# Optimization experiments

Hardware: AMD Instinct MI355X
Metric: run time of the kernel (lower is better)

## Reference

```python
import jax, jax.numpy as jnp
import numpy as np

BETA = 0.25

def setup_inputs() -> dict:
    key = jax.random.key(0)
    k1, k2 = jax.random.split(key)
    x = jax.random.normal(k1, (32, 32, 32, 64), dtype=jnp.float32)
    # tf.random_uniform_initializer default: uniform in [-0.05, 0.05]
    embeddings = jax.random.uniform(k2, (64, 1024), dtype=jnp.float32,
                                    minval=-0.05, maxval=0.05)
    return {"x": x, "embeddings": embeddings}

def reference(x, embeddings):
    D, K = embeddings.shape
    flat = x.reshape(-1, D)                                   # [N, D]
    # squared L2 distances to each codebook vector (expanded form)
    sim = flat @ embeddings                                   # [N, K]
    dists = (jnp.sum(flat * flat, axis=1, keepdims=True)
             + jnp.sum(embeddings * embeddings, axis=0)
             - 2.0 * sim)                                     # [N, K]
    idx = jnp.argmin(dists, axis=1)                           # [N]
    quantized = embeddings.T[idx].reshape(x.shape)            # gather == one-hot matmul
    commitment_loss = BETA * jnp.mean((jax.lax.stop_gradient(quantized) - x) ** 2)
    codebook_loss = jnp.mean((quantized - jax.lax.stop_gradient(x)) ** 2)
    loss = commitment_loss + codebook_loss
    out = x + jax.lax.stop_gradient(quantized - x)            # straight-through
    return out, loss
```

## Files before the change

### kernel.cpp

```cpp
#include <hip/hip_runtime.h>
#include <hip/hip_bf16.h>


#define NROWS 32768
#define DDIM  64
#define KCODE 1024
#define NELEM (NROWS * DDIM)
#define MARGIN 4e-3f
#define FIXBLOCKS 256
#define MAINBLK 256

typedef __attribute__((ext_vector_type(8))) _Float16 f16x8;
typedef __attribute__((ext_vector_type(4))) float f32x4;

static __device__ __forceinline__ unsigned short f2h(float v) {
    _Float16 h = (_Float16)v;
    unsigned short b;
    __builtin_memcpy(&b, &h, 2);
    return b;
}
static __device__ __forceinline__ void gload16(const void* g, void* l) {
    __builtin_amdgcn_global_load_lds(
        (const __attribute__((address_space(1))) void*)g,
        (__attribute__((address_space(3))) void*)l, 16, 0, 0);
}

__global__ void vq_prep(const float* __restrict__ e,
                        float* __restrict__ se,
                        float* __restrict__ eT,
                        unsigned short* __restrict__ ehSw,
                        int* __restrict__ ctrl) {
    __shared__ float tile[64][17];
    const int t = threadIdx.x;
    const int k0 = blockIdx.x * 16;
    if (blockIdx.x == 0 && t < 4) ctrl[t] = 0;
    #pragma unroll
    for (int i = 0; i < 4; ++i) {
        int idx = i * 256 + t;
        int d = idx >> 4, kk = idx & 15;
        tile[d][kk] = e[d * KCODE + k0 + kk];
    }
    __syncthreads();
    if (t < 16) {
        float s = 0.f;
        #pragma unroll
        for (int d = 0; d < 64; ++d) { float v = tile[d][t]; s = fmaf(v, v, s); }
        se[k0 + t] = s;
    }
    const int kk = t >> 4;
    const int dg = (t & 15) * 4;
    const int kg = k0 + kk;
    float v0 = tile[dg + 0][kk], v1 = tile[dg + 1][kk];
    float v2 = tile[dg + 2][kk], v3 = tile[dg + 3][kk];
    *(float4*)&eT[(size_t)kg * 64 + dg] = make_float4(v0, v1, v2, v3);
    const int sw = (((dg >> 3) ^ (kg & 7)) << 3) + (dg & 7);
    *(ushort4*)&ehSw[(size_t)kg * 64 + sw] =
        make_ushort4(f2h(v0), f2h(v1), f2h(v2), f2h(v3));
}

__launch_bounds__(512)
__global__ void vq_main(const float* __restrict__ x,
                        const float* __restrict__ se,
                        const float* __restrict__ eT,
                        const unsigned short* __restrict__ ehSw,
                        float* __restrict__ out,
                        float* __restrict__ parts,
                        int* __restrict__ cnt,
                        int2* __restrict__ list) {
    __shared__ unsigned short Beh[KCODE * 64];
    __shared__ float sse[KCODE];
    __shared__ float wsum[8];

    const int t = threadIdx.x;
    const int lane = t & 63;
    const int w = t >> 6;
    const int quad = lane >> 4, l15 = lane & 15;
    const int rowBase = blockIdx.x * 128 + w * 16;

    {
        const unsigned char* g = (const unsigned char*)ehSw;
        #pragma unroll
        for (int r = 0; r < 16; ++r)
            gload16(g + (size_t)(r * 512 + t) * 16, &Beh[(r * 512 + t) * 8]);
        float2 s2 = ((const float2*)se)[t];
        sse[2 * t + 0] = s2.x;
        sse[2 * t + 1] = s2.y;
    }

    f16x8 ah0, ah1, al0, al1;
    {
        const float4* ap0 = (const float4*)(x + (size_t)(rowBase + l15) * 64 + quad * 8);
        const float4* ap1 = (const float4*)(x + (size_t)(rowBase + l15) * 64 + 32 + quad * 8);
        float4 a0 = ap0[0], a1 = ap0[1], b0 = ap1[0], b1 = ap1[1];
        float av[8] = {a0.x, a0.y, a0.z, a0.w, a1.x, a1.y, a1.z, a1.w};
        float bv[8] = {b0.x, b0.y, b0.z, b0.w, b1.x, b1.y, b1.z, b1.w};
        f16x8 h0, h1, l0, l1;
        #pragma unroll
        for (int j = 0; j < 8; ++j) {
            _Float16 ha = (_Float16)av[j];
            _Float16 hb = (_Float16)bv[j];
            h0[j] = ha;
            h1[j] = hb;
            l0[j] = (_Float16)(av[j] - (float)ha);
            l1[j] = (_Float16)(bv[j] - (float)hb);
        }
        ah0 = h0; ah1 = h1; al0 = l0; al1 = l1;
    }
    __syncthreads();

    float sb[4], sb2[4];
    int   si[4];
    #pragma unroll
    for (int r = 0; r < 4; ++r) { sb[r] = 3.4e38f; sb2[r] = 3.4e38f; si[r] = 0; }

    const int slot0 = ((quad ^ (l15 & 7)) << 3);
    const int slot1 = (((quad + 4) ^ (l15 & 7)) << 3);

    #pragma unroll 4
    for (int nt = 0; nt < 64; ++nt) {
        const int code = nt * 16 + l15;
        f16x8 b0 = *(const f16x8*)&Beh[code * 64 + slot0];
        f16x8 b1 = *(const f16x8*)&Beh[code * 64 + slot1];
        float cse = sse[code];
        f32x4 aA = {0.f, 0.f, 0.f, 0.f}, aB = {0.f, 0.f, 0.f, 0.f};
        aA = __builtin_amdgcn_mfma_f32_16x16x32_f16(ah0, b0, aA, 0, 0, 0);
        aB = __builtin_amdgcn_mfma_f32_16x16x32_f16(ah1, b1, aB, 0, 0, 0);
        aA = __builtin_amdgcn_mfma_f32_16x16x32_f16(al0, b0, aA, 0, 0, 0);
        aB = __builtin_amdgcn_mfma_f32_16x16x32_f16(al1, b1, aB, 0, 0, 0);
        #pragma unroll
        for (int r = 0; r < 4; ++r) {
            float key = fmaf(-2.f, aA[r] + aB[r], cse);
            bool lt = key < sb[r];
            sb2[r] = fminf(sb2[r], fmaxf(sb[r], key));
            sb[r]  = fminf(sb[r], key);
            si[r]  = lt ? code : si[r];
        }
    }

    #pragma unroll
    for (int m = 1; m < 16; m <<= 1) {
        #pragma unroll
        for (int r = 0; r < 4; ++r) {
            float ob  = __shfl_xor(sb[r],  m, 64);
            float ob2 = __shfl_xor(sb2[r], m, 64);
            int   oi  = __shfl_xor(si[r],  m, 64);
            float nb2 = fminf(fminf(sb2[r], ob2), fmaxf(sb[r], ob));
            bool take = (ob < sb[r]) || (ob == sb[r] && oi < si[r]);
            sb[r] = take ? ob : sb[r];
            si[r] = take ? oi : si[r];
            sb2[r] = nb2;
        }
    }

    if (l15 == 0) {
        #pragma unroll
        for (int r = 0; r < 4; ++r) {
            if (sb2[r] - sb[r] < MARGIN) {
                int p = atomicAdd(cnt, 1);
                list[p] = make_int2(rowBase + quad * 4 + r, si[r]);
            }
        }
    }

    int src = (l15 >> 2) << 4;
    int j0 = __shfl(si[0], src, 64);
    int j1 = __shfl(si[1], src, 64);
    int j2 = __shfl(si[2], src, 64);
    int j3 = __shfl(si[3], src, 64);
    int rsel = l15 & 3;
    int myidx = rsel == 0 ? j0 : (rsel == 1 ? j1 : (rsel == 2 ? j2 : j3));

    {
        const float4* qrow = (const float4*)(eT + (size_t)myidx * 64 + quad * 16);
        const float4* xrow = (const float4*)(x + (size_t)(rowBase + l15) * 64 + quad * 16);
        float4* orow = (float4*)(out + (size_t)(rowBase + l15) * 64 + quad * 16);
        float lsum = 0.f;
        #pragma unroll
        for (int i = 0; i < 4; ++i) {
            float4 q = qrow[i];
            float4 xv = xrow[i];
            float4 o;
            float dx;
            dx = q.x - xv.x; o.x = xv.x + dx; lsum = fmaf(dx, dx, lsum);
            dx = q.y - xv.y; o.y = xv.y + dx; lsum = fmaf(dx, dx, lsum);
            dx = q.z - xv.z; o.z = xv.z + dx; lsum = fmaf(dx, dx, lsum);
            dx = q.w - xv.w; o.w = xv.w + dx; lsum = fmaf(dx, dx, lsum);
            orow[i] = o;
        }
        #pragma unroll
        for (int off = 32; off > 0; off >>= 1)
            lsum += __shfl_down(lsum, off, 64);
        if (lane == 0) wsum[w] = lsum;
    }
    __syncthreads();
    if (t == 0) {
        float s = 0.f;
        #pragma unroll
        for (int i = 0; i < 8; ++i) s += wsum[i];
        parts[blockIdx.x] = s;
    }
}

__launch_bounds__(256)
__global__ void vq_fix(const float* __restrict__ x,
                       const float* __restrict__ se,
                       const float* __restrict__ eT,
                       const int2* __restrict__ list,
                       const int* __restrict__ cnt,
                       const float* __restrict__ parts,
                       float* __restrict__ lossAcc,
                       int* __restrict__ done,
                       float* __restrict__ out) {
    __shared__ float xs[64];
    __shared__ float cb[256];
    __shared__ int   ci[256];
    __shared__ int   newIdxS;
    __shared__ int   lastS;
    const int t = threadIdx.x;
    const int n = *cnt;

    for (int i = blockIdx.x; i < n; i += gridDim.x) {
        int2 en = list[i];
        const int row = en.x, oldIdx = en.y;
        if (t < 64) xs[t] = x[(size_t)row * 64 + t];
        __syncthreads();

        float sx = 0.f;
        #pragma unroll
        for (int d = 0; d < 64; ++d) sx = fmaf(xs[d], xs[d], sx);

        const int k0 = t * 4;
        const float4* e0 = (const float4*)(eT + (size_t)(k0 + 0) * 64);
        const float4* e1 = (const float4*)(eT + (size_t)(k0 + 1) * 64);
        const float4* e2 = (const float4*)(eT + (size_t)(k0 + 2) * 64);
        const float4* e3 = (const float4*)(eT + (size_t)(k0 + 3) * 64);
        float dot0 = 0.f, dot1 = 0.f, dot2 = 0.f, dot3 = 0.f;
        #pragma unroll
        for (int i4 = 0; i4 < 16; ++i4) {
            float4 v0 = e0[i4], v1 = e1[i4], v2 = e2[i4], v3 = e3[i4];
            float xa = xs[4 * i4 + 0], xb = xs[4 * i4 + 1];
            float xc = xs[4 * i4 + 2], xd = xs[4 * i4 + 3];
            dot0 = fmaf(xa, v0.x, dot0); dot0 = fmaf(xb, v0.y, dot0);
            dot0 = fmaf(xc, v0.z, dot0); dot0 = fmaf(xd, v0.w, dot0);
            dot1 = fmaf(xa, v1.x, dot1); dot1 = fmaf(xb, v1.y, dot1);
            dot1 = fmaf(xc, v1.z, dot1); dot1 = fmaf(xd, v1.w, dot1);
            dot2 = fmaf(xa, v2.x, dot2); dot2 = fmaf(xb, v2.y, dot2);
            dot2 = fmaf(xc, v2.z, dot2); dot2 = fmaf(xd, v2.w, dot2);
            dot3 = fmaf(xa, v3.x, dot3); dot3 = fmaf(xb, v3.y, dot3);
            dot3 = fmaf(xc, v3.z, dot3); dot3 = fmaf(xd, v3.w, dot3);
        }
        float dd0 = (sx + se[k0 + 0]) - 2.0f * dot0;
        float dd1 = (sx + se[k0 + 1]) - 2.0f * dot1;
        float dd2 = (sx + se[k0 + 2]) - 2.0f * dot2;
        float dd3 = (sx + se[k0 + 3]) - 2.0f * dot3;
        float db = dd0; int di = k0;
        if (dd1 < db) { db = dd1; di = k0 + 1; }
        if (dd2 < db) { db = dd2; di = k0 + 2; }
        if (dd3 < db) { db = dd3; di = k0 + 3; }
        cb[t] = db; ci[t] = di;
        __syncthreads();

        if (t < 64) {
            float B = cb[t]; int I = ci[t];
            #pragma unroll
            for (int s = 64; s < 256; s += 64) {
                float b = cb[t + s]; int i2 = ci[t + s];
                bool take = (b < B) || (b == B && i2 < I);
                B = take ? b : B;
                I = take ? i2 : I;
            }
            #pragma unroll
            for (int m = 1; m < 64; m <<= 1) {
                float ob = __shfl_xor(B, m, 64);
                int   oi = __shfl_xor(I, m, 64);
                bool take = (ob < B) || (ob == B && oi < I);
                B = take ? ob : B;
                I = take ? oi : I;
            }
            if (t == 0) newIdxS = I;
        }
        __syncthreads();

        const int ni = newIdxS;
        if (ni != oldIdx) {
            if (t < 64) {
                float xv = xs[t];
                float qn = eT[(size_t)ni * 64 + t];
                float qo = eT[(size_t)oldIdx * 64 + t];
                float dn = qn - xv, dl = qo - xv;
                out[(size_t)row * 64 + t] = xv + dn;
                float delta = dn * dn - dl * dl;
                #pragma unroll
                for (int off = 32; off > 0; off >>= 1)
                    delta += __shfl_down(delta, off, 64);
                if (t == 0) atomicAdd(lossAcc, delta);
            }
        }
        __syncthreads();
    }

    if (t == 0) {
        __threadfence();
        int fin = atomicAdd(done, 1);
        lastS = (fin == FIXBLOCKS - 1) ? 1 : 0;
    }
    __syncthreads();
    if (lastS) {
        cb[t] = parts[t];
        __syncthreads();
        if (t < 64) {
            float v = cb[t] + cb[t + 64] + cb[t + 128] + cb[t + 192];
            #pragma unroll
            for (int off = 32; off > 0; off >>= 1)
                v += __shfl_down(v, off, 64);
            if (t == 0) {
                float total = v + atomicAdd(lossAcc, 0.0f);
                float m = total / (float)NELEM;
                out[NELEM] = 0.25f * m + m;
            }
        }
    }
}

extern "C" void kernel_launch(void* const* d_in, const int* in_sizes, int n_in,
                              void* d_out, int out_size, void* d_ws, size_t ws_size,
                              hipStream_t stream) {
    const float* x = (const float*)d_in[0];
    const float* e = (const float*)d_in[1];
    float* out = (float*)d_out;
    float* ws  = (float*)d_ws;

    float* lossAcc       = ws;
    int*   cnt           = (int*)(ws + 1);
    int*   done          = (int*)(ws + 2);
    float* se            = ws + 64;
    float* eT            = ws + 1280;
    unsigned short* ehSw = (unsigned short*)(ws + 66816);
    int2*  list          = (int2*)(ws + 99584);
    float* parts         = ws + 165120;

    vq_prep<<<64, 256, 0, stream>>>(e, se, eT, ehSw, (int*)ws);
    vq_main<<<MAINBLK, 512, 0, stream>>>(x, se, eT, ehSw, out, parts, cnt, list);
    vq_fix<<<FIXBLOCKS, 256, 0, stream>>>(x, se, eT, list, cnt, parts, lossAcc, done, out);
}
```

Before: 107.7 us.

## Fuse fp32 rescoring of ambiguous rows into main kernel, drop fix kernel

Ambiguous rows, where the fp16 top-2 gap is under the margin, are now rescored exactly in fp32 inside the main kernel. Each block keeps a shared-memory list of its flagged rows and resolves them before writing outputs, so the per-row write happens once with the final index. The separate fix kernel launch, the global atomic list and the loss-delta correction all go away. The cost is that flagged rows are handled serially within each block, with block-wide syncs per row, which may cause imbalance across blocks.

```diff
diff --git a/kernel.cpp b/kernel.cpp
--- a/kernel.cpp
+++ b/kernel.cpp
@@ -7,7 +7,6 @@
 #define KCODE 1024
 #define NELEM (NROWS * DDIM)
 #define MARGIN 4e-3f
-#define FIXBLOCKS 256
 #define MAINBLK 256
 
 typedef __attribute__((ext_vector_type(8))) _Float16 f16x8;
@@ -65,17 +64,26 @@
                         const unsigned short* __restrict__ ehSw,
                         float* __restrict__ out,
                         float* __restrict__ parts,
-                        int* __restrict__ cnt,
-                        int2* __restrict__ list) {
+                        int* __restrict__ done) {
     __shared__ unsigned short Beh[KCODE * 64];
     __shared__ float sse[KCODE];
+    __shared__ float cbuf[512];
+    __shared__ int   cibuf[512];
+    __shared__ int   rowIdx[128];
+    __shared__ int   flagRows[128];
+    __shared__ int   nFlag;
+    __shared__ float xs[64];
     __shared__ float wsum[8];
+    __shared__ int   lastS;
 
     const int t = threadIdx.x;
     const int lane = t & 63;
     const int w = t >> 6;
     const int quad = lane >> 4, l15 = lane & 15;
-    const int rowBase = blockIdx.x * 128 + w * 16;
+    const int rowBlk = blockIdx.x * 128;
+    const int rowBase = rowBlk + w * 16;
+
+    if (t == 0) { nFlag = 0; lastS = 0; }
 
     {
         const unsigned char* g = (const unsigned char*)ehSw;
@@ -155,23 +163,74 @@
     if (l15 == 0) {
         #pragma unroll
         for (int r = 0; r < 4; ++r) {
+            const int rl = w * 16 + quad * 4 + r;
+            rowIdx[rl] = si[r];
             if (sb2[r] - sb[r] < MARGIN) {
-                int p = atomicAdd(cnt, 1);
-                list[p] = make_int2(rowBase + quad * 4 + r, si[r]);
-            }
-        }
-    }
-
-    int src = (l15 >> 2) << 4;
-    int j0 = __shfl(si[0], src, 64);
-    int j1 = __shfl(si[1], src, 64);
-    int j2 = __shfl(si[2], src, 64);
-    int j3 = __shfl(si[3], src, 64);
-    int rsel = l15 & 3;
-    int myidx = rsel == 0 ? j0 : (rsel == 1 ? j1 : (rsel == 2 ? j2 : j3));
-
-    {
-        const float4* qrow = (const float4*)(eT + (size_t)myidx * 64 + quad * 16);
+                int p = atomicAdd(&nFlag, 1);
+                flagRows[p] = rl;
+            }
+        }
+    }
+    __syncthreads();
+
+    {
+        const int nf = nFlag;
+        for (int f = 0; f < nf; ++f) {
+            const int r = flagRows[f];
+            if (t < 64) xs[t] = x[(size_t)(rowBlk + r) * 64 + t];
+            __syncthreads();
+
+            float sx = 0.f;
+            #pragma unroll
+            for (int d = 0; d < 64; ++d) sx = fmaf(xs[d], xs[d], sx);
+
+            const int k0 = t * 2;
+            const float4* e0 = (const float4*)(eT + (size_t)(k0 + 0) * 64);
+            const float4* e1 = (const float4*)(eT + (size_t)(k0 + 1) * 64);
+            float dot0 = 0.f, dot1 = 0.f;
+            #pragma unroll
+            for (int i4 = 0; i4 < 16; ++i4) {
+                float4 v0 = e0[i4], v1 = e1[i4];
+                float xa = xs[4 * i4 + 0], xb = xs[4 * i4 + 1];
+                float xc = xs[4 * i4 + 2], xd = xs[4 * i4 + 3];
+                dot0 = fmaf(xa, v0.x, dot0); dot0 = fmaf(xb, v0.y, dot0);
+                dot0 = fmaf(xc, v0.z, dot0); dot0 = fmaf(xd, v0.w, dot0);
+                dot1 = fmaf(xa, v1.x, dot1); dot1 = fmaf(xb, v1.y, dot1);
+                dot1 = fmaf(xc, v1.z, dot1); dot1 = fmaf(xd, v1.w, dot1);
+            }
+            float dd0 = (sx + sse[k0 + 0]) - 2.0f * dot0;
+            float dd1 = (sx + sse[k0 + 1]) - 2.0f * dot1;
+            float db = dd0; int di = k0;
+            if (dd1 < db) { db = dd1; di = k0 + 1; }
+            cbuf[t] = db; cibuf[t] = di;
+            __syncthreads();
+
+            if (t < 64) {
+                float B = cbuf[t]; int I = cibuf[t];
+                #pragma unroll
+                for (int s = 64; s < 512; s += 64) {
+                    float b = cbuf[t + s]; int i2 = cibuf[t + s];
+                    bool take = (b < B) || (b == B && i2 < I);
+                    B = take ? b : B;
+                    I = take ? i2 : I;
+                }
+                #pragma unroll
+                for (int m = 1; m < 64; m <<= 1) {
+                    float ob = __shfl_xor(B, m, 64);
+                    int   oi = __shfl_xor(I, m, 64);
+                    bool take = (ob < B) || (ob == B && oi < I);
+                    B = take ? ob : B;
+                    I = take ? oi : I;
+                }
+                if (t == 0) rowIdx[r] = I;
+            }
+            __syncthreads();
+        }
+    }
+
+    {
+        const int idx = rowIdx[w * 16 + l15];
+        const float4* qrow = (const float4*)(eT + (size_t)idx * 64 + quad * 16);
         const float4* xrow = (const float4*)(x + (size_t)(rowBase + l15) * 64 + quad * 16);
         float4* orow = (float4*)(out + (size_t)(rowBase + l15) * 64 + quad * 16);
         float lsum = 0.f;
@@ -193,129 +252,27 @@
         if (lane == 0) wsum[w] = lsum;
     }
     __syncthreads();
+
     if (t == 0) {
         float s = 0.f;
         #pragma unroll
         for (int i = 0; i < 8; ++i) s += wsum[i];
         parts[blockIdx.x] = s;
-    }
-}
-
-__launch_bounds__(256)
-__global__ void vq_fix(const float* __restrict__ x,
-                       const float* __restrict__ se,
-                       const float* __restrict__ eT,
-                       const int2* __restrict__ list,
-                       const int* __restrict__ cnt,
-                       const float* __restrict__ parts,
-                       float* __restrict__ lossAcc,
-                       int* __restrict__ done,
-                       float* __restrict__ out) {
-    __shared__ float xs[64];
-    __shared__ float cb[256];
-    __shared__ int   ci[256];
-    __shared__ int   newIdxS;
-    __shared__ int   lastS;
-    const int t = threadIdx.x;
-    const int n = *cnt;
-
-    for (int i = blockIdx.x; i < n; i += gridDim.x) {
-        int2 en = list[i];
-        const int row = en.x, oldIdx = en.y;
-        if (t < 64) xs[t] = x[(size_t)row * 64 + t];
-        __syncthreads();
-
-        float sx = 0.f;
-        #pragma unroll
-        for (int d = 0; d < 64; ++d) sx = fmaf(xs[d], xs[d], sx);
-
-        const int k0 = t * 4;
-        const float4* e0 = (const float4*)(eT + (size_t)(k0 + 0) * 64);
-        const float4* e1 = (const float4*)(eT + (size_t)(k0 + 1) * 64);
-        const float4* e2 = (const float4*)(eT + (size_t)(k0 + 2) * 64);
-        const float4* e3 = (const float4*)(eT + (size_t)(k0 + 3) * 64);
-        float dot0 = 0.f, dot1 = 0.f, dot2 = 0.f, dot3 = 0.f;
-        #pragma unroll
-        for (int i4 = 0; i4 < 16; ++i4) {
-            float4 v0 = e0[i4], v1 = e1[i4], v2 = e2[i4], v3 = e3[i4];
-            float xa = xs[4 * i4 + 0], xb = xs[4 * i4 + 1];
-            float xc = xs[4 * i4 + 2], xd = xs[4 * i4 + 3];
-            dot0 = fmaf(xa, v0.x, dot0); dot0 = fmaf(xb, v0.y, dot0);
-            dot0 = fmaf(xc, v0.z, dot0); dot0 = fmaf(xd, v0.w, dot0);
-            dot1 = fmaf(xa, v1.x, dot1); dot1 = fmaf(xb, v1.y, dot1);
-            dot1 = fmaf(xc, v1.z, dot1); dot1 = fmaf(xd, v1.w, dot1);
-            dot2 = fmaf(xa, v2.x, dot2); dot2 = fmaf(xb, v2.y, dot2);
-            dot2 = fmaf(xc, v2.z, dot2); dot2 = fmaf(xd, v2.w, dot2);
-            dot3 = fmaf(xa, v3.x, dot3); dot3 = fmaf(xb, v3.y, dot3);
-            dot3 = fmaf(xc, v3.z, dot3); dot3 = fmaf(xd, v3.w, dot3);
-        }
-        float dd0 = (sx + se[k0 + 0]) - 2.0f * dot0;
-        float dd1 = (sx + se[k0 + 1]) - 2.0f * dot1;
-        float dd2 = (sx + se[k0 + 2]) - 2.0f * dot2;
-        float dd3 = (sx + se[k0 + 3]) - 2.0f * dot3;
-        float db = dd0; int di = k0;
-        if (dd1 < db) { db = dd1; di = k0 + 1; }
-        if (dd2 < db) { db = dd2; di = k0 + 2; }
-        if (dd3 < db) { db = dd3; di = k0 + 3; }
-        cb[t] = db; ci[t] = di;
-        __syncthreads();
-
-        if (t < 64) {
-            float B = cb[t]; int I = ci[t];
-            #pragma unroll
-            for (int s = 64; s < 256; s += 64) {
-                float b = cb[t + s]; int i2 = ci[t + s];
-                bool take = (b < B) || (b == B && i2 < I);
-                B = take ? b : B;
-                I = take ? i2 : I;
-            }
-            #pragma unroll
-            for (int m = 1; m < 64; m <<= 1) {
-                float ob = __shfl_xor(B, m, 64);
-                int   oi = __shfl_xor(I, m, 64);
-                bool take = (ob < B) || (ob == B && oi < I);
-                B = take ? ob : B;
-                I = take ? oi : I;
-            }
-            if (t == 0) newIdxS = I;
-        }
-        __syncthreads();
-
-        const int ni = newIdxS;
-        if (ni != oldIdx) {
-            if (t < 64) {
-                float xv = xs[t];
-                float qn = eT[(size_t)ni * 64 + t];
-                float qo = eT[(size_t)oldIdx * 64 + t];
-                float dn = qn - xv, dl = qo - xv;
-                out[(size_t)row * 64 + t] = xv + dn;
-                float delta = dn * dn - dl * dl;
-                #pragma unroll
-                for (int off = 32; off > 0; off >>= 1)
-                    delta += __shfl_down(delta, off, 64);
-                if (t == 0) atomicAdd(lossAcc, delta);
-            }
-        }
-        __syncthreads();
-    }
-
-    if (t == 0) {
         __threadfence();
         int fin = atomicAdd(done, 1);
-        lastS = (fin == FIXBLOCKS - 1) ? 1 : 0;
+        if (fin == MAINBLK - 1) lastS = 1;
     }
     __syncthreads();
     if (lastS) {
-        cb[t] = parts[t];
+        if (t < 256) cbuf[t] = parts[t];
         __syncthreads();
         if (t < 64) {
-            float v = cb[t] + cb[t + 64] + cb[t + 128] + cb[t + 192];
+            float v = cbuf[t] + cbuf[t + 64] + cbuf[t + 128] + cbuf[t + 192];
             #pragma unroll
             for (int off = 32; off > 0; off >>= 1)
                 v += __shfl_down(v, off, 64);
             if (t == 0) {
-                float total = v + atomicAdd(lossAcc, 0.0f);
-                float m = total / (float)NELEM;
+                float m = v / (float)NELEM;
                 out[NELEM] = 0.25f * m + m;
             }
         }
@@ -330,16 +287,12 @@
     float* out = (float*)d_out;
     float* ws  = (float*)d_ws;
 
-    float* lossAcc       = ws;
-    int*   cnt           = (int*)(ws + 1);
     int*   done          = (int*)(ws + 2);
     float* se            = ws + 64;
     float* eT            = ws + 1280;
     unsigned short* ehSw = (unsigned short*)(ws + 66816);
-    int2*  list          = (int2*)(ws + 99584);
-    float* parts         = ws + 165120;
+    float* parts         = ws + 99584;
 
     vq_prep<<<64, 256, 0, stream>>>(e, se, eT, ehSw, (int*)ws);
-    vq_main<<<MAINBLK, 512, 0, stream>>>(x, se, eT, ehSw, out, parts, cnt, list);
-    vq_fix<<<FIXBLOCKS, 256, 0, stream>>>(x, se, eT, list, cnt, parts, lossAcc, done, out);
-}
+    vq_main<<<MAINBLK, 512, 0, stream>>>(x, se, eT, ehSw, out, parts, done);
+}
```

New measurement: 109.5 us. Within noise of the previous version (+1.7%).
